# Kernel tuning notes

Hardware: AMD Instinct MI355X
Metric: run time of the kernel (lower is better)

Reference implementation:

```python
import jax, jax.numpy as jnp
import numpy as np

B, T, D = 2, 2048, 1024
H, DH, P = 16, 64, 512


def setup_inputs() -> dict:
    key = jax.random.key(0)
    ks = jax.random.split(key, 7)
    s = 0.02
    return {
        "x": jax.random.normal(ks[0], (B, T, D), jnp.float32),
        "prefix_k": jax.random.normal(ks[1], (B, H, P, DH), jnp.float32),
        "prefix_v": jax.random.normal(ks[2], (B, H, P, DH), jnp.float32),
        "Wq": jax.random.normal(ks[3], (D, D), jnp.float32) * s,
        "Wk": jax.random.normal(ks[4], (D, D), jnp.float32) * s,
        "Wv": jax.random.normal(ks[5], (D, D), jnp.float32) * s,
        "Wo": jax.random.normal(ks[6], (D, D), jnp.float32) * s,
    }


def reference(x, prefix_k, prefix_v, Wq, Wk, Wv, Wo):
    b, t, c = x.shape
    h, dh = H, DH
    # nn.Linear without bias: y = x @ W.T
    q = (x @ Wq.T).reshape(b, t, h, dh).transpose(0, 2, 1, 3)  # [B,H,T,Dh]
    k = (x @ Wk.T).reshape(b, t, h, dh).transpose(0, 2, 1, 3)
    v = (x @ Wv.T).reshape(b, t, h, dh).transpose(0, 2, 1, 3)
    k = jnp.concatenate([prefix_k, k], axis=2)  # [B,H,P+T,Dh]
    v = jnp.concatenate([prefix_v, v], axis=2)
    scale = 1.0 / jnp.sqrt(jnp.float32(dh))
    att = jnp.einsum("bhqd,bhkd->bhqk", q, k) * scale  # [B,H,T,P+T]
    att = jax.nn.softmax(att, axis=-1)  # no causal mask in source
    y = jnp.einsum("bhqk,bhkd->bhqd", att, v)  # [B,H,T,Dh]
    y = y.transpose(0, 2, 1, 3).reshape(b, t, c)
    return y @ Wo.T
```

## Files before the change

### kernel.cpp

```cpp
#include <hip/hip_runtime.h>
#include <cstdint>

#define Bv  2
#define Tv  2048
#define Dv  1024
#define Hv  16
#define DHv 64
#define Pv  512
#define Lv  2560

typedef __attribute__((ext_vector_type(8))) short sh8;
typedef __attribute__((ext_vector_type(4))) short sh4;
typedef __attribute__((ext_vector_type(4))) float f4;
typedef __attribute__((ext_vector_type(4))) unsigned int u4v;

#define MFMA(a,b,c) __builtin_amdgcn_mfma_f32_16x16x32_bf16(a,b,c,0,0,0)

__device__ __forceinline__ unsigned short bf16_rn(float f) {
    unsigned int u = __builtin_bit_cast(unsigned int, f);
    u += 0x7FFFu + ((u >> 16) & 1u);
    return (unsigned short)(u >> 16);
}
__device__ __forceinline__ float bf16_f(unsigned short h) {
    unsigned int u = ((unsigned int)h) << 16;
    return __builtin_bit_cast(float, u);
}
__device__ __forceinline__ unsigned int fbits(float f) {
    return __builtin_bit_cast(unsigned int, f);
}

__device__ __forceinline__ void gload16(const unsigned short* g, unsigned short* l) {
    __builtin_amdgcn_global_load_lds(
        (const __attribute__((address_space(1))) unsigned int*)(g),
        (__attribute__((address_space(3))) unsigned int*)(l),
        16, 0, 0);
}

__device__ __forceinline__ sh8 packP(const f4 a, const f4 b) {
    float e0 = __builtin_amdgcn_exp2f(a[0]), e1 = __builtin_amdgcn_exp2f(a[1]);
    float e2 = __builtin_amdgcn_exp2f(a[2]), e3 = __builtin_amdgcn_exp2f(a[3]);
    float f0 = __builtin_amdgcn_exp2f(b[0]), f1 = __builtin_amdgcn_exp2f(b[1]);
    float f2 = __builtin_amdgcn_exp2f(b[2]), f3 = __builtin_amdgcn_exp2f(b[3]);
    u4v d;
    d[0] = __builtin_amdgcn_perm(fbits(e1), fbits(e0), 0x07060302u);
    d[1] = __builtin_amdgcn_perm(fbits(e3), fbits(e2), 0x07060302u);
    d[2] = __builtin_amdgcn_perm(fbits(f1), fbits(f0), 0x07060302u);
    d[3] = __builtin_amdgcn_perm(fbits(f3), fbits(f2), 0x07060302u);
    return __builtin_bit_cast(sh8, d);
}

__global__ __launch_bounds__(256) void prep_convert(
    const float* __restrict__ x,  const float* __restrict__ Wq,
    const float* __restrict__ Wk, const float* __restrict__ Wv,
    const float* __restrict__ pk, const float* __restrict__ Wo,
    unsigned short* __restrict__ xb,  unsigned short* __restrict__ wqb,
    unsigned short* __restrict__ wkb, unsigned short* __restrict__ wvb,
    unsigned short* __restrict__ pkb, unsigned short* __restrict__ woh,
    unsigned short* __restrict__ wol)
{
    int i = blockIdx.x * 256 + threadIdx.x;
    const float* src; unsigned short* dst; int off; bool split = false;
    if      (i < 1048576) { src = x;  dst = xb;  off = i; }
    else if (i < 1310720) { src = Wq; dst = wqb; off = i - 1048576; }
    else if (i < 1572864) { src = Wk; dst = wkb; off = i - 1310720; }
    else if (i < 1835008) { src = Wv; dst = wvb; off = i - 1572864; }
    else if (i < 2097152) { src = pk; dst = pkb; off = i - 1835008; }
    else                  { src = Wo; dst = woh; off = i - 2097152; split = true; }
    float4 v = reinterpret_cast<const float4*>(src)[off];
    float vv[4] = {v.x, v.y, v.z, v.w};
    sh4 h, l;
    #pragma unroll
    for (int j = 0; j < 4; j++) {
        unsigned short hh = bf16_rn(vv[j]);
        h[j] = (short)hh;
        l[j] = (short)bf16_rn(vv[j] - bf16_f(hh));
    }
    reinterpret_cast<sh4*>(dst)[off] = h;
    if (split) reinterpret_cast<sh4*>(wol)[off] = l;
}

__global__ __launch_bounds__(256) void prep_transpose(
    const float* __restrict__ pv, unsigned short* __restrict__ pvtb)
{
    __shared__ unsigned short Tls[64][66];
    const int tid = threadIdx.x;
    const int bh = blockIdx.x >> 3, pt = blockIdx.x & 7;
    #pragma unroll
    for (int i = 0; i < 4; i++) {
        int id = i * 256 + tid;
        int p = id >> 4, c4 = (id & 15) << 2;
        float4 v = *reinterpret_cast<const float4*>(
            &pv[((size_t)bh * Pv + pt * 64 + p) * DHv + c4]);
        Tls[c4+0][p] = bf16_rn(v.x);
        Tls[c4+1][p] = bf16_rn(v.y);
        Tls[c4+2][p] = bf16_rn(v.z);
        Tls[c4+3][p] = bf16_rn(v.w);
    }
    __syncthreads();
    #pragma unroll
    for (int i = 0; i < 2; i++) {
        int id = i * 256 + tid;
        int d = id >> 3, u = id & 7;
        sh4 lo, hi;
        #pragma unroll
        for (int j = 0; j < 4; j++) {
            lo[j] = (short)Tls[d][u * 8 + j];
            hi[j] = (short)Tls[d][u * 8 + 4 + j];
        }
        int p0 = ((u >> 2) & 1) * 32 + (u & 1) * 16 + ((u >> 1) & 1) * 4;
        size_t base = ((size_t)bh * DHv + d) * Pv + pt * 64;
        *reinterpret_cast<sh4*>(&pvtb[base + p0])     = lo;
        *reinterpret_cast<sh4*>(&pvtb[base + p0 + 8]) = hi;
    }
}

__global__ __launch_bounds__(256) void qkv_gemm(
    const unsigned short* __restrict__ xb,
    const unsigned short* __restrict__ wqb, const unsigned short* __restrict__ wkb,
    const unsigned short* __restrict__ wvb,
    unsigned short* __restrict__ qb, unsigned short* __restrict__ kb,
    unsigned short* __restrict__ vtb)
{
    __shared__ __align__(16) unsigned short As[128 * 64], Bs[128 * 64];
    const int tid = threadIdx.x;
    const int lane = tid & 63, w = tid >> 6;
    const int g = lane >> 4, tx = lane & 15;
    const int wr = w >> 1, wc = w & 1;
    const int m0 = blockIdx.x * 128, n0 = blockIdx.y * 128;
    const int z = blockIdx.z;
    const unsigned short* Wb = (z == 0) ? wqb : (z == 1) ? wkb : wvb;
    const int srow = lane >> 3, scol = lane & 7;

    f4 acc[4][4] = {};

    for (int k0 = 0; k0 < Dv; k0 += 64) {
        #pragma unroll
        for (int c = 0; c < 4; c++) {
            int row = w * 32 + c * 8 + srow;
            int su = (scol ^ (row & 7)) << 3;
            gload16(&xb[(size_t)(m0 + row) * Dv + k0 + su], &As[(w * 32 + c * 8) * 64]);
            gload16(&Wb[(size_t)(n0 + row) * Dv + k0 + su], &Bs[(w * 32 + c * 8) * 64]);
        }
        __syncthreads();
        #pragma unroll
        for (int ks = 0; ks < 2; ks++) {
            sh8 fa[4], fb[4];
            #pragma unroll
            for (int mi = 0; mi < 4; mi++) {
                int r = wr * 64 + mi * 16 + tx;
                fa[mi] = *reinterpret_cast<const sh8*>(&As[(r * 64 + ks * 32 + g * 8) ^ ((r & 7) << 3)]);
            }
            #pragma unroll
            for (int ni = 0; ni < 4; ni++) {
                int r = wc * 64 + ni * 16 + tx;
                fb[ni] = *reinterpret_cast<const sh8*>(&Bs[(r * 64 + ks * 32 + g * 8) ^ ((r & 7) << 3)]);
            }
            if (z < 2) {
                #pragma unroll
                for (int mi = 0; mi < 4; mi++)
                    #pragma unroll
                    for (int ni = 0; ni < 4; ni++)
                        acc[mi][ni] = MFMA(fb[ni], fa[mi], acc[mi][ni]);
            } else {
                #pragma unroll
                for (int mi = 0; mi < 4; mi++)
                    #pragma unroll
                    for (int ni = 0; ni < 4; ni++)
                        acc[mi][ni] = MFMA(fa[mi], fb[ni], acc[mi][ni]);
            }
        }
        __syncthreads();
    }

    if (z < 2) {
        unsigned short* ob = (z == 0) ? qb : kb;
        const float sc = (z == 0) ? 0.1803368801f : 1.0f;
        #pragma unroll
        for (int mi = 0; mi < 4; mi++)
            #pragma unroll
            for (int ni = 0; ni < 4; ni++) {
                int m = m0 + wr * 64 + mi * 16 + tx;
                int n = n0 + wc * 64 + ni * 16 + g * 4;
                sh4 pkd;
                #pragma unroll
                for (int i = 0; i < 4; i++) pkd[i] = (short)bf16_rn(acc[mi][ni][i] * sc);
                *reinterpret_cast<sh4*>(&ob[(size_t)m * Dv + n]) = pkd;
            }
    } else {
        const int tb0 = ((m0 + wr * 64) & (Tv - 1));
        const int b   = (m0 + wr * 64) >> 11;
        #pragma unroll
        for (int mi = 0; mi < 4; mi++)
            #pragma unroll
            for (int ni = 0; ni < 4; ni++) {
                int t = tb0 + ((mi & 2) << 4) + (g << 3) + ((mi & 1) << 2);
                int n = n0 + wc * 64 + ni * 16 + tx;
                int h = n >> 6, dh = n & 63;
                sh4 pkd;
                #pragma unroll
                for (int i = 0; i < 4; i++) pkd[i] = (short)bf16_rn(acc[mi][ni][i]);
                *reinterpret_cast<sh4*>(&vtb[(((size_t)(b * Hv + h)) * DHv + dh) * Tv + t]) = pkd;
            }
    }
}

__global__ __launch_bounds__(256) void flash_mfma(
    const unsigned short* __restrict__ qbuf, const unsigned short* __restrict__ kb,
    const unsigned short* __restrict__ vtb,
    const unsigned short* __restrict__ pkb, const unsigned short* __restrict__ pvtb,
    unsigned short* __restrict__ yh, unsigned short* __restrict__ yl)
{
    __shared__ __align__(16) unsigned short Ks[2][64 * 64], Vs[2][64 * 64];
    __shared__ float olex[2][4][64];
    const int tid = threadIdx.x;
    const int lane = tid & 63, w = tid >> 6;
    const int kw = w & 1, qw = w >> 1;
    const int g = lane >> 4, tx = lane & 15;
    const int pblk = blockIdx.x;
    const int L = (pblk & 7) * 64 + (pblk >> 3);
    const int qt = L & 15;
    const int bh = L >> 4;
    const int b = bh >> 4, h = bh & 15;
    const int srow = lane >> 3, scol = lane & 7;

    sh8 qf[4][2];
    #pragma unroll
    for (int qg = 0; qg < 4; qg++) {
        size_t base = ((size_t)(b * Tv) + qt * 128 + qw * 64 + qg * 16 + tx) * Dv + h * 64;
        qf[qg][0] = *reinterpret_cast<const sh8*>(&qbuf[base + g * 8]);
        qf[qg][1] = *reinterpret_cast<const sh8*>(&qbuf[base + 32 + g * 8]);
    }

    f4 o[4][4] = {};
    f4 ol[4] = {};
    sh8 onesf;
    #pragma unroll
    for (int j = 0; j < 8; j++) onesf[j] = (short)0x3F80;

    const int r0 = w * 16 + srow, r1 = r0 + 8;
    const int su0 = (scol ^ (r0 & 7)) << 3;
    const int su1 = (scol ^ (r1 & 7)) << 3;
    const unsigned short* ka0 = &pkb[((size_t)bh * Pv + r0) * DHv + su0];
    const unsigned short* ka1 = &pkb[((size_t)bh * Pv + r1) * DHv + su1];
    const unsigned short* va0 = &pvtb[((size_t)bh * DHv + r0) * Pv + su0];
    const unsigned short* va1 = &pvtb[((size_t)bh * DHv + r1) * Pv + su1];

    auto stage = [&](int buf) {
        gload16(ka0, &Ks[buf][(w * 16    ) * 64]);
        gload16(ka1, &Ks[buf][(w * 16 + 8) * 64]);
        gload16(va0, &Vs[buf][(w * 16    ) * 64]);
        gload16(va1, &Vs[buf][(w * 16 + 8) * 64]);
    };
    auto advance = [&](int nt) {
        if (nt == 7) {
            ka0 = &kb[((size_t)(b * Tv) + r0) * Dv + h * 64 + su0];
            ka1 = &kb[((size_t)(b * Tv) + r1) * Dv + h * 64 + su1];
            va0 = &vtb[((size_t)bh * DHv + r0) * Tv + su0];
            va1 = &vtb[((size_t)bh * DHv + r1) * Tv + su1];
        } else if (nt < 7) { ka0 += 64 * DHv; ka1 += 64 * DHv; va0 += 64; va1 += 64; }
        else               { ka0 += 64 * Dv;  ka1 += 64 * Dv;  va0 += 64; va1 += 64; }
    };

    stage(0); advance(0);
    __syncthreads();
    int cur = 0;

    for (int t = 0; t < Lv / 64; t++) {
        if (t + 1 < Lv / 64) { stage(cur ^ 1); advance(t + 1); }

        sh8 kf[2][2], vf[4];
        #pragma unroll
        for (int nf = 0; nf < 2; nf++) {
            int rk = 32 * kw + nf * 16 + tx;
            kf[nf][0] = *reinterpret_cast<const sh8*>(
                &Ks[cur][(rk * 64 + g * 8) ^ ((rk & 7) << 3)]);
            kf[nf][1] = *reinterpret_cast<const sh8*>(
                &Ks[cur][(rk * 64 + 32 + g * 8) ^ ((rk & 7) << 3)]);
        }
        #pragma unroll
        for (int nf = 0; nf < 4; nf++) {
            int rv = nf * 16 + tx;
            vf[nf] = *reinterpret_cast<const sh8*>(
                &Vs[cur][(rv * 64 + 32 * kw + g * 8) ^ ((rv & 7) << 3)]);
        }

        #pragma unroll
        for (int qg = 0; qg < 4; qg++) {
            f4 sa = {}, sb = {};
            sa = MFMA(kf[0][0], qf[qg][0], sa); sa = MFMA(kf[0][1], qf[qg][1], sa);
            sb = MFMA(kf[1][0], qf[qg][0], sb); sb = MFMA(kf[1][1], qf[qg][1], sb);
            sh8 pf = packP(sa, sb);
            #pragma unroll
            for (int nf = 0; nf < 4; nf++)
                o[qg][nf] = MFMA(vf[nf], pf, o[qg][nf]);
            ol[qg] = MFMA(onesf, pf, ol[qg]);
        }
        __syncthreads();
        cur ^= 1;
    }

    float* ex = qw ? reinterpret_cast<float*>(Vs) : reinterpret_cast<float*>(Ks);
    if (kw) {
        #pragma unroll
        for (int qg = 0; qg < 4; qg++) {
            #pragma unroll
            for (int nf = 0; nf < 4; nf++)
                *reinterpret_cast<f4*>(&ex[((qg * 4 + nf) * 64 + lane) * 4]) = o[qg][nf];
            olex[qw][qg][lane] = ol[qg][0];
        }
    }
    __syncthreads();
    if (!kw) {
        #pragma unroll
        for (int qg = 0; qg < 4; qg++) {
            float l = ol[qg][0] + olex[qw][qg][lane];
            float inv = 1.0f / l;
            size_t ybase = ((size_t)(b * Tv) + qt * 128 + qw * 64 + qg * 16 + tx) * Dv + h * 64;
            #pragma unroll
            for (int nf = 0; nf < 4; nf++) {
                f4 op = o[qg][nf] +
                    *reinterpret_cast<const f4*>(&ex[((qg * 4 + nf) * 64 + lane) * 4]);
                sh4 ph, pl;
                #pragma unroll
                for (int i = 0; i < 4; i++) {
                    float v = op[i] * inv;
                    unsigned short hh = bf16_rn(v);
                    ph[i] = (short)hh;
                    pl[i] = (short)bf16_rn(v - bf16_f(hh));
                }
                *reinterpret_cast<sh4*>(&yh[ybase + nf * 16 + g * 4]) = ph;
                *reinterpret_cast<sh4*>(&yl[ybase + nf * 16 + g * 4]) = pl;
            }
        }
    }
}

__global__ __launch_bounds__(256) void out_gemm(
    const unsigned short* __restrict__ yh, const unsigned short* __restrict__ yl,
    const unsigned short* __restrict__ woh, const unsigned short* __restrict__ wol,
    float* __restrict__ out)
{
    __shared__ __align__(16) unsigned short As[64 * 64], Bs[128 * 64];
    const int tid = threadIdx.x;
    const int lane = tid & 63, w = tid >> 6;
    const int g = lane >> 4, tx = lane & 15;
    const int wr = w >> 1, wc = w & 1;
    const int m0 = blockIdx.x * 64, n0 = blockIdx.y * 128;
    const int srow = lane >> 3, scol = lane & 7;

    f4 acc[2][4] = {};

    for (int k0 = 0; k0 < 3 * Dv; k0 += 64) {
        int seg = k0 >> 10, kk = k0 & (Dv - 1);
        const unsigned short* Asrc = (seg == 1) ? yl : yh;
        const unsigned short* Bsrc = (seg == 2) ? wol : woh;
        #pragma unroll
        for (int c = 0; c < 2; c++) {
            int row = w * 16 + c * 8 + srow;
            int su = (scol ^ (row & 7)) << 3;
            gload16(&Asrc[(size_t)(m0 + row) * Dv + kk + su], &As[(w * 16 + c * 8) * 64]);
        }
        #pragma unroll
        for (int c = 0; c < 4; c++) {
            int row = w * 32 + c * 8 + srow;
            int su = (scol ^ (row & 7)) << 3;
            gload16(&Bsrc[(size_t)(n0 + row) * Dv + kk + su], &Bs[(w * 32 + c * 8) * 64]);
        }
        __syncthreads();
        #pragma unroll
        for (int ks = 0; ks < 2; ks++) {
            sh8 fa[2], fb[4];
            #pragma unroll
            for (int mi = 0; mi < 2; mi++) {
                int r = wr * 32 + mi * 16 + tx;
                fa[mi] = *reinterpret_cast<const sh8*>(&As[(r * 64 + ks * 32 + g * 8) ^ ((r & 7) << 3)]);
            }
            #pragma unroll
            for (int ni = 0; ni < 4; ni++) {
                int r = wc * 64 + ni * 16 + tx;
                fb[ni] = *reinterpret_cast<const sh8*>(&Bs[(r * 64 + ks * 32 + g * 8) ^ ((r & 7) << 3)]);
            }
            #pragma unroll
            for (int mi = 0; mi < 2; mi++)
                #pragma unroll
                for (int ni = 0; ni < 4; ni++)
                    acc[mi][ni] = MFMA(fb[ni], fa[mi], acc[mi][ni]);
        }
        __syncthreads();
    }

    #pragma unroll
    for (int mi = 0; mi < 2; mi++)
        #pragma unroll
        for (int ni = 0; ni < 4; ni++) {
            int m = m0 + wr * 32 + mi * 16 + tx;
            int n = n0 + wc * 64 + ni * 16 + g * 4;
            *reinterpret_cast<float4*>(&out[(size_t)m * Dv + n]) =
                make_float4(acc[mi][ni][0], acc[mi][ni][1], acc[mi][ni][2], acc[mi][ni][3]);
        }
}

extern "C" void kernel_launch(void* const* d_in, const int* in_sizes, int n_in,
                              void* d_out, int out_size, void* d_ws, size_t ws_size,
                              hipStream_t stream)
{
    const float* x  = (const float*)d_in[0];
    const float* pk = (const float*)d_in[1];
    const float* pv = (const float*)d_in[2];
    const float* Wq = (const float*)d_in[3];
    const float* Wk = (const float*)d_in[4];
    const float* Wv = (const float*)d_in[5];
    const float* Wo = (const float*)d_in[6];

    const size_t M1 = 1048576;
    unsigned short* ws  = (unsigned short*)d_ws;
    unsigned short* xb   = ws;
    unsigned short* wqb  = ws + 4  * M1;
    unsigned short* wkb  = ws + 5  * M1;
    unsigned short* wvb  = ws + 6  * M1;
    unsigned short* woh  = ws + 7  * M1;
    unsigned short* wol  = ws + 8  * M1;
    unsigned short* pkb  = ws + 9  * M1;
    unsigned short* pvtb = ws + 10 * M1;
    unsigned short* qb   = ws + 11 * M1;
    unsigned short* kb   = ws + 15 * M1;
    unsigned short* vtb  = ws + 19 * M1;
    unsigned short* yh   = ws + 23 * M1;
    unsigned short* yl   = ws + 27 * M1;

    prep_convert<<<9216, 256, 0, stream>>>(x, Wq, Wk, Wv, pk, Wo,
                                           xb, wqb, wkb, wvb, pkb, woh, wol);
    prep_transpose<<<256, 256, 0, stream>>>(pv, pvtb);
    qkv_gemm<<<dim3(32, 8, 3), 256, 0, stream>>>(xb, wqb, wkb, wvb, qb, kb, vtb);
    flash_mfma<<<dim3(Bv * Hv * (Tv / 128)), 256, 0, stream>>>(qb, kb, vtb, pkb, pvtb, yh, yl);
    out_gemm<<<dim3(64, 8), 256, 0, stream>>>(yh, yl, woh, wol, (float*)d_out);
}
```

Before: 150.0 us.

## Drop split-bf16 output projection and hand-pipeline flash attention loads

Removes the hi/lo bf16 split of the attention output and Wo, so the output GEMM runs one bf16 pass over K=1024 instead of three. This also drops the extra yl and wol buffers and the stores that fill them. Separately, the flash attention loop is restructured with explicit s_waitcnt vmcnt and s_barrier plus sched_barriers, so the next tile's loads overlap the current compute with finer-grained waits. The precision drop lowers the accuracy of the final projection, which could threaten the tolerance check.

```diff
diff --git a/kernel.cpp b/kernel.cpp
--- a/kernel.cpp
+++ b/kernel.cpp
@@ -55,28 +55,21 @@
     const float* __restrict__ pk, const float* __restrict__ Wo,
     unsigned short* __restrict__ xb,  unsigned short* __restrict__ wqb,
     unsigned short* __restrict__ wkb, unsigned short* __restrict__ wvb,
-    unsigned short* __restrict__ pkb, unsigned short* __restrict__ woh,
-    unsigned short* __restrict__ wol)
+    unsigned short* __restrict__ pkb, unsigned short* __restrict__ woh)
 {
     int i = blockIdx.x * 256 + threadIdx.x;
-    const float* src; unsigned short* dst; int off; bool split = false;
+    const float* src; unsigned short* dst; int off;
     if      (i < 1048576) { src = x;  dst = xb;  off = i; }
     else if (i < 1310720) { src = Wq; dst = wqb; off = i - 1048576; }
     else if (i < 1572864) { src = Wk; dst = wkb; off = i - 1310720; }
     else if (i < 1835008) { src = Wv; dst = wvb; off = i - 1572864; }
     else if (i < 2097152) { src = pk; dst = pkb; off = i - 1835008; }
-    else                  { src = Wo; dst = woh; off = i - 2097152; split = true; }
+    else                  { src = Wo; dst = woh; off = i - 2097152; }
     float4 v = reinterpret_cast<const float4*>(src)[off];
-    float vv[4] = {v.x, v.y, v.z, v.w};
-    sh4 h, l;
-    #pragma unroll
-    for (int j = 0; j < 4; j++) {
-        unsigned short hh = bf16_rn(vv[j]);
-        h[j] = (short)hh;
-        l[j] = (short)bf16_rn(vv[j] - bf16_f(hh));
-    }
+    sh4 h;
+    h[0] = (short)bf16_rn(v.x); h[1] = (short)bf16_rn(v.y);
+    h[2] = (short)bf16_rn(v.z); h[3] = (short)bf16_rn(v.w);
     reinterpret_cast<sh4*>(dst)[off] = h;
-    if (split) reinterpret_cast<sh4*>(wol)[off] = l;
 }
 
 __global__ __launch_bounds__(256) void prep_transpose(
@@ -208,7 +201,7 @@
     const unsigned short* __restrict__ qbuf, const unsigned short* __restrict__ kb,
     const unsigned short* __restrict__ vtb,
     const unsigned short* __restrict__ pkb, const unsigned short* __restrict__ pvtb,
-    unsigned short* __restrict__ yh, unsigned short* __restrict__ yl)
+    unsigned short* __restrict__ yh)
 {
     __shared__ __align__(16) unsigned short Ks[2][64 * 64], Vs[2][64 * 64];
     __shared__ float olex[2][4][64];
@@ -261,13 +254,7 @@
         else               { ka0 += 64 * Dv;  ka1 += 64 * Dv;  va0 += 64; va1 += 64; }
     };
 
-    stage(0); advance(0);
-    __syncthreads();
-    int cur = 0;
-
-    for (int t = 0; t < Lv / 64; t++) {
-        if (t + 1 < Lv / 64) { stage(cur ^ 1); advance(t + 1); }
-
+    auto compute = [&](int cur) {
         sh8 kf[2][2], vf[4];
         #pragma unroll
         for (int nf = 0; nf < 2; nf++) {
@@ -283,7 +270,6 @@
             vf[nf] = *reinterpret_cast<const sh8*>(
                 &Vs[cur][(rv * 64 + 32 * kw + g * 8) ^ ((rv & 7) << 3)]);
         }
-
         #pragma unroll
         for (int qg = 0; qg < 4; qg++) {
             f4 sa = {}, sb = {};
@@ -295,9 +281,28 @@
                 o[qg][nf] = MFMA(vf[nf], pf, o[qg][nf]);
             ol[qg] = MFMA(onesf, pf, ol[qg]);
         }
-        __syncthreads();
+    };
+
+    stage(0); advance(0);
+    asm volatile("s_waitcnt vmcnt(0)" ::: "memory");
+    __builtin_amdgcn_s_barrier();
+    __builtin_amdgcn_sched_barrier(0);
+    int cur = 0;
+
+    for (int t = 0; t < Lv / 64 - 1; t++) {
+        stage(cur ^ 1); advance(t + 1);
+        asm volatile("s_waitcnt vmcnt(4)" ::: "memory");
+        __builtin_amdgcn_s_barrier();
+        __builtin_amdgcn_sched_barrier(0);
+        compute(cur);
+        __builtin_amdgcn_sched_barrier(0);
+        __builtin_amdgcn_s_barrier();
         cur ^= 1;
     }
+    asm volatile("s_waitcnt vmcnt(0)" ::: "memory");
+    __builtin_amdgcn_s_barrier();
+    __builtin_amdgcn_sched_barrier(0);
+    compute(cur);
 
     float* ex = qw ? reinterpret_cast<float*>(Vs) : reinterpret_cast<float*>(Ks);
     if (kw) {
@@ -320,24 +325,18 @@
             for (int nf = 0; nf < 4; nf++) {
                 f4 op = o[qg][nf] +
                     *reinterpret_cast<const f4*>(&ex[((qg * 4 + nf) * 64 + lane) * 4]);
-                sh4 ph, pl;
-                #pragma unroll
-                for (int i = 0; i < 4; i++) {
-                    float v = op[i] * inv;
-                    unsigned short hh = bf16_rn(v);
-                    ph[i] = (short)hh;
-                    pl[i] = (short)bf16_rn(v - bf16_f(hh));
-                }
+                sh4 ph;
+                #pragma unroll
+                for (int i = 0; i < 4; i++) ph[i] = (short)bf16_rn(op[i] * inv);
                 *reinterpret_cast<sh4*>(&yh[ybase + nf * 16 + g * 4]) = ph;
-                *reinterpret_cast<sh4*>(&yl[ybase + nf * 16 + g * 4]) = pl;
             }
         }
     }
 }
 
 __global__ __launch_bounds__(256) void out_gemm(
-    const unsigned short* __restrict__ yh, const unsigned short* __restrict__ yl,
-    const unsigned short* __restrict__ woh, const unsigned short* __restrict__ wol,
+    const unsigned short* __restrict__ yh,
+    const unsigned short* __restrict__ woh,
     float* __restrict__ out)
 {
     __shared__ __align__(16) unsigned short As[64 * 64], Bs[128 * 64];
@@ -350,21 +349,18 @@
 
     f4 acc[2][4] = {};
 
-    for (int k0 = 0; k0 < 3 * Dv; k0 += 64) {
-        int seg = k0 >> 10, kk = k0 & (Dv - 1);
-        const unsigned short* Asrc = (seg == 1) ? yl : yh;
-        const unsigned short* Bsrc = (seg == 2) ? wol : woh;
+    for (int k0 = 0; k0 < Dv; k0 += 64) {
         #pragma unroll
         for (int c = 0; c < 2; c++) {
             int row = w * 16 + c * 8 + srow;
             int su = (scol ^ (row & 7)) << 3;
-            gload16(&Asrc[(size_t)(m0 + row) * Dv + kk + su], &As[(w * 16 + c * 8) * 64]);
+            gload16(&yh[(size_t)(m0 + row) * Dv + k0 + su], &As[(w * 16 + c * 8) * 64]);
         }
         #pragma unroll
         for (int c = 0; c < 4; c++) {
             int row = w * 32 + c * 8 + srow;
             int su = (scol ^ (row & 7)) << 3;
-            gload16(&Bsrc[(size_t)(n0 + row) * Dv + kk + su], &Bs[(w * 32 + c * 8) * 64]);
+            gload16(&woh[(size_t)(n0 + row) * Dv + k0 + su], &Bs[(w * 32 + c * 8) * 64]);
         }
         __syncthreads();
         #pragma unroll
@@ -419,19 +415,17 @@
     unsigned short* wkb  = ws + 5  * M1;
     unsigned short* wvb  = ws + 6  * M1;
     unsigned short* woh  = ws + 7  * M1;
-    unsigned short* wol  = ws + 8  * M1;
-    unsigned short* pkb  = ws + 9  * M1;
-    unsigned short* pvtb = ws + 10 * M1;
-    unsigned short* qb   = ws + 11 * M1;
-    unsigned short* kb   = ws + 15 * M1;
-    unsigned short* vtb  = ws + 19 * M1;
-    unsigned short* yh   = ws + 23 * M1;
-    unsigned short* yl   = ws + 27 * M1;
+    unsigned short* pkb  = ws + 8  * M1;
+    unsigned short* pvtb = ws + 9  * M1;
+    unsigned short* qb   = ws + 10 * M1;
+    unsigned short* kb   = ws + 14 * M1;
+    unsigned short* vtb  = ws + 18 * M1;
+    unsigned short* yh   = ws + 22 * M1;
 
     prep_convert<<<9216, 256, 0, stream>>>(x, Wq, Wk, Wv, pk, Wo,
-                                           xb, wqb, wkb, wvb, pkb, woh, wol);
+                                           xb, wqb, wkb, wvb, pkb, woh);
     prep_transpose<<<256, 256, 0, stream>>>(pv, pvtb);
     qkv_gemm<<<dim3(32, 8, 3), 256, 0, stream>>>(xb, wqb, wkb, wvb, qb, kb, vtb);
-    flash_mfma<<<dim3(Bv * Hv * (Tv / 128)), 256, 0, stream>>>(qb, kb, vtb, pkb, pvtb, yh, yl);
-    out_gemm<<<dim3(64, 8), 256, 0, stream>>>(yh, yl, woh, wol, (float*)d_out);
-}
+    flash_mfma<<<dim3(Bv * Hv * (Tv / 128)), 256, 0, stream>>>(qb, kb, vtb, pkb, pvtb, yh);
+    out_gemm<<<dim3(64, 8), 256, 0, stream>>>(yh, woh, (float*)d_out);
+}
```

Measured after the change: 121.0 us. 19.3% less time.
